# Kernel tuning notes

Measured on AMD Instinct MI355X. Metric: run time of the kernel, lower is better.

The kernel has to match this reference:

```python
import jax, jax.numpy as jnp
import numpy as np

NUM_FEAT = 1024
NUM_GROUP = 16
DIM_K = NUM_FEAT // NUM_GROUP  # 64
FEAT_DIM = 64
WAVE_LENGTH = 1000.0


def position_embedding(box, ctx_box):
    # box: (M,4), ctx_box: (N,4) corner encoding -> (M*N, 64)
    xmin, ymin, xmax, ymax = jnp.split(box, 4, axis=1)            # (M,1) each
    bw = xmax - xmin + 1.0
    bh = ymax - ymin + 1.0
    cx = 0.5 * (xmin + xmax)
    cy = 0.5 * (ymin + ymax)
    cxmin, cymin, cxmax, cymax = jnp.split(ctx_box, 4, axis=1)    # (N,1) each
    cbw = cxmax - cxmin + 1.0
    cbh = cymax - cymin + 1.0
    ccx = 0.5 * (cxmin + cxmax)
    ccy = 0.5 * (cymin + cymax)
    dx = jnp.log(jnp.clip(jnp.abs((cx - ccx.T) / bw), 1e-3))      # (M,N)
    dy = jnp.log(jnp.clip(jnp.abs((cy - ccy.T) / bh), 1e-3))
    dw = jnp.log(cbw.T / bw)
    dh = jnp.log(cbh.T / bh)
    pos = jnp.stack((dx, dy, dw, dh), axis=2)                     # (M,N,4)
    feat_range = jnp.arange(FEAT_DIM // 8, dtype=jnp.float32)     # (8,)
    dim_mat = jnp.power(jnp.float32(WAVE_LENGTH), (8.0 / FEAT_DIM) * feat_range)
    div = (100.0 * pos)[..., None] / dim_mat                      # (M,N,4,8)
    emb = jnp.concatenate((jnp.sin(div), jnp.cos(div)), axis=3)   # (M,N,4,16)
    M, N = pos.shape[0], pos.shape[1]
    return emb.reshape(M * N, FEAT_DIM)


def setup_inputs() -> dict:
    key = jax.random.key(0)
    ks = jax.random.split(key, 12)
    M, N = 512, 1024

    def make_boxes(k, n):
        k1, k2 = jax.random.split(k)
        xy = jax.random.uniform(k1, (n, 2), dtype=jnp.float32) * 800.0
        wh = jax.random.uniform(k2, (n, 2), dtype=jnp.float32) * 200.0 + 1.0
        return jnp.concatenate([xy, xy + wh], axis=1)             # valid corners

    return {
        "feat": jax.random.normal(ks[0], (M, NUM_FEAT), dtype=jnp.float32),
        "ctx_feat": jax.random.normal(ks[1], (N, NUM_FEAT), dtype=jnp.float32),
        "box": make_boxes(ks[2], M),
        "ctx_box": make_boxes(ks[3], N),
        # torch Linear stores weight as (out, in); apply as x @ W.T + b
        "w_fc_gt": jax.random.normal(ks[4], (NUM_FEAT, 1024), dtype=jnp.float32) * 0.01,
        "b_fc_gt": jnp.zeros((NUM_FEAT,), dtype=jnp.float32),
        "w_fc_ctx": jax.random.normal(ks[5], (NUM_FEAT, 1024), dtype=jnp.float32) * 0.01,
        "b_fc_ctx": jnp.zeros((NUM_FEAT,), dtype=jnp.float32),
        "w_pos_gt": jax.random.normal(ks[6], (NUM_GROUP, FEAT_DIM), dtype=jnp.float32) * 0.01,
        "b_pos_gt": jnp.zeros((NUM_GROUP,), dtype=jnp.float32),
        "w_pos_ctx": jax.random.normal(ks[7], (NUM_GROUP, FEAT_DIM), dtype=jnp.float32) * 0.01,
        "b_pos_ctx": jnp.zeros((NUM_GROUP,), dtype=jnp.float32),
        # grouped 1x1 conv (16384 -> 1024, groups=16): per-group weight (64 out, 1024 in)
        "w_conv": jax.random.normal(ks[8], (NUM_GROUP, DIM_K, NUM_FEAT), dtype=jnp.float32) * 0.02,
        "b_conv": jnp.zeros((NUM_FEAT,), dtype=jnp.float32),
    }


def reference(feat, ctx_feat, box, ctx_box,
              w_fc_gt, b_fc_gt, w_fc_ctx, b_fc_ctx,
              w_pos_gt, b_pos_gt, w_pos_ctx, b_pos_ctx,
              w_conv, b_conv):
    M, N = feat.shape[0], ctx_feat.shape[0]
    # positional bias per group: (M*N,64) -relu-> linear -> (G,M,N)
    pe_gt = jax.nn.relu(position_embedding(box, ctx_box))
    pos_gt = (pe_gt @ w_pos_gt.T + b_pos_gt).T.reshape(NUM_GROUP, M, N)
    pe_ctx = jax.nn.relu(position_embedding(ctx_box, box))
    pos_ctx = (pe_ctx @ w_pos_ctx.T + b_pos_ctx).T.reshape(NUM_GROUP, N, M)
    # grouped projections
    q = (feat @ w_fc_gt.T + b_fc_gt).reshape(M, NUM_GROUP, DIM_K)
    k = (ctx_feat @ w_fc_ctx.T + b_fc_ctx).reshape(N, NUM_GROUP, DIM_K)
    scores = jnp.einsum('mgd,ngd->gmn', q, k) / np.float32(np.sqrt(DIM_K))  # (G,M,N)
    # gt <- ctx attention with log-position bias
    w1 = jax.nn.softmax(jnp.log(jnp.clip(pos_gt, 1e-6)) + scores, axis=-1)  # (G,M,N)
    att1 = jnp.einsum('gmn,nc->mgc', w1, ctx_feat)                          # (M,G,1024)
    out_gt = jnp.einsum('mgc,goc->mgo', att1, w_conv).reshape(M, NUM_FEAT) + b_conv
    # ctx <- gt attention (note: original module reuses gt_ctx_linear_out here)
    w2 = jax.nn.softmax(jnp.log(jnp.clip(pos_ctx, 1e-6)) + scores.transpose(0, 2, 1), axis=-1)  # (G,N,M)
    att2 = jnp.einsum('gnm,mc->ngc', w2, feat)                              # (N,G,1024)
    out_ctx = jnp.einsum('ngc,goc->ngo', att2, w_conv).reshape(N, NUM_FEAT) + b_conv
    return out_gt, out_ctx
```

## Files before the change

### kernel.cpp

```cpp
#include <hip/hip_runtime.h>
#include <math.h>


typedef __attribute__((ext_vector_type(8))) short short8;
typedef __attribute__((ext_vector_type(4))) float floatx4;
typedef __attribute__((ext_vector_type(4))) _Float16 half4;
typedef __attribute__((ext_vector_type(4))) unsigned uint4v;

__device__ inline unsigned short f32_bf16_rne(float x) {
    union { float f; unsigned u; } v; v.f = x;
    unsigned u = v.u;
    return (unsigned short)((u + 0x7fffu + ((u >> 16) & 1u)) >> 16);
}

__device__ inline unsigned fbits(float x) {
    union { float f; unsigned u; } v; v.f = x; return v.u;
}
__device__ inline float bitsf(unsigned u) {
    union { unsigned u; float f; } v; v.u = u; return v.f;
}

__device__ __forceinline__ floatx4 mfma16(short8 a, short8 b, floatx4 c) {
    return __builtin_amdgcn_mfma_f32_16x16x32_bf16(a, b, c, 0, 0, 0);
}

__device__ __forceinline__ void gemm_tile_pack(
    const unsigned short* __restrict__ Ab, int lda,
    const unsigned short* __restrict__ Bb, int ldb, int K,
    unsigned short* __restrict__ out_base,
    const float* __restrict__ biasvec,
    unsigned short* As, unsigned short* Bs)
{
    const int tid = threadIdx.x;
    const int lr = tid >> 3;
    const int lk = (tid & 7) * 8;
    const int lane = tid & 63;
    const int wave = tid >> 6;
    const int qr = (wave >> 1) * 32;
    const int qc = (wave & 1) * 32;
    const int m = lane & 15;
    const int quad = lane >> 4;

    const unsigned short* Ap  = Ab + (long long)lr * lda + lk;
    const unsigned short* Ap2 = Ap + 32LL * lda;
    const unsigned short* Bp  = Bb + (long long)lr * ldb + lk;
    const unsigned short* Bp2 = Bp + 32LL * ldb;
    unsigned short* AsW  = As + lr * 72 + lk;
    unsigned short* AsW2 = As + (lr + 32) * 72 + lk;
    unsigned short* BsW  = Bs + lr * 72 + lk;
    unsigned short* BsW2 = Bs + (lr + 32) * 72 + lk;
    const unsigned short* a0p = As + (qr + m) * 72 + quad * 8;
    const unsigned short* b0p = Bs + (qc + m) * 72 + quad * 8;

    floatx4 acc00 = {0.f,0.f,0.f,0.f}, acc01 = {0.f,0.f,0.f,0.f};
    floatx4 acc10 = {0.f,0.f,0.f,0.f}, acc11 = {0.f,0.f,0.f,0.f};

    int4 pa0 = *(const int4*)Ap;
    int4 pa1 = *(const int4*)Ap2;
    int4 pb0 = *(const int4*)Bp;
    int4 pb1 = *(const int4*)Bp2;
    int4 qa0 = *(const int4*)(Ap + 64);
    int4 qa1 = *(const int4*)(Ap2 + 64);
    int4 qb0 = *(const int4*)(Bp + 64);
    int4 qb1 = *(const int4*)(Bp2 + 64);

    for (int k0 = 0; ; ) {
        __syncthreads();
        *(int4*)AsW  = pa0;
        *(int4*)AsW2 = pa1;
        *(int4*)BsW  = pb0;
        *(int4*)BsW2 = pb1;
        __syncthreads();
        pa0 = qa0; pa1 = qa1; pb0 = qb0; pb1 = qb1;
        const int kf = k0 + 128;
        if (kf < K) {
            qa0 = *(const int4*)(Ap + kf);
            qa1 = *(const int4*)(Ap2 + kf);
            qb0 = *(const int4*)(Bp + kf);
            qb1 = *(const int4*)(Bp2 + kf);
        }
        #pragma unroll
        for (int kk = 0; kk < 64; kk += 32) {
            short8 a0 = *(const short8*)(a0p + kk);
            short8 a1 = *(const short8*)(a0p + 16 * 72 + kk);
            short8 b0 = *(const short8*)(b0p + kk);
            short8 b1 = *(const short8*)(b0p + 16 * 72 + kk);
            acc00 = mfma16(a0, b0, acc00);
            acc01 = mfma16(a0, b1, acc01);
            acc10 = mfma16(a1, b0, acc10);
            acc11 = mfma16(a1, b1, acc11);
        }
        k0 += 64;
        if (k0 >= K) break;
    }

    float bias0 = 0.f, bias1 = 0.f;
    if (biasvec) { bias0 = biasvec[qc + m]; bias1 = biasvec[qc + 16 + m]; }

    __syncthreads();
    const floatx4 accs[2][2] = { {acc00, acc01}, {acc10, acc11} };
    #pragma unroll
    for (int i = 0; i < 2; ++i)
        #pragma unroll
        for (int r = 0; r < 4; ++r) {
            const int lrow = qr + i * 16 + quad * 4 + r;
            #pragma unroll
            for (int j = 0; j < 2; ++j) {
                const int lcol = qc + j * 16 + m;
                float val = accs[i][j][r] + (j ? bias1 : bias0);
                As[lrow * 72 + lcol] = f32_bf16_rne(val);
            }
        }
    __syncthreads();
    #pragma unroll
    for (int h = 0; h < 2; ++h) {
        const int f = h * 2048 + tid * 8;
        const int lanep = (f >> 3) & 63;
        const int part = (f >> 9) & 1;
        const int ploc = f >> 10;
        const int row = ploc * 16 + (lanep & 15);
        const int col = part * 32 + ((lanep >> 4) << 3);
        short8 v8 = *(const short8*)&As[row * 72 + col];
        *(short8*)(out_base + f) = v8;
    }
}

__global__ __launch_bounds__(256) void projvt_kernel(
    const unsigned short* __restrict__ in_bf, const unsigned short* __restrict__ wgt,
    const unsigned short* __restrict__ wctx,
    const float* __restrict__ bgt, const float* __restrict__ bctx,
    unsigned short* __restrict__ qk_pack,
    const unsigned short* __restrict__ wconv, unsigned short* __restrict__ vt_pack)
{
    __shared__ __align__(16) unsigned short As[64 * 72];
    __shared__ __align__(16) unsigned short Bs[64 * 72];
    if (blockIdx.z == 0) {
        const int bm = blockIdx.x * 64;
        const int g = blockIdx.y;
        const unsigned short* B = (bm < 512) ? wgt : wctx;
        const float* bias = (bm < 512) ? bgt : bctx;
        gemm_tile_pack(in_bf + (long long)bm * 1024, 1024,
                       B + (long long)g * 65536, 1024, 1024,
                       qk_pack + ((long long)g * 96 + blockIdx.x * 4) * 1024,
                       bias + g * 64, As, Bs);
    } else {
        const int cc = blockIdx.x;
        const int g = blockIdx.y;
        gemm_tile_pack(wconv + (long long)g * 65536, 1024,
                       in_bf + (long long)cc * 65536, 1024, 1024,
                       vt_pack + ((long long)g * 24 + cc) * 4096,
                       nullptr, As, Bs);
    }
}

__global__ __launch_bounds__(256) void prep_kernel(
    const float* __restrict__ box, const float* __restrict__ ctx_box,
    const float* __restrict__ w_gt, const float* __restrict__ b_gt,
    const float* __restrict__ w_ctx, const float* __restrict__ b_ctx,
    _Float16* __restrict__ bias_gt, _Float16* __restrict__ bias_ctx,
    const float* s0, unsigned short* d0, int n0,
    const float* s1, unsigned short* d1, int n1,
    const float* s2, unsigned short* d2, int n2,
    const float* s3, unsigned short* d3, int n3,
    const float* s4, unsigned short* d4, int n4)
{
    const int bx = blockIdx.x;
    if (bx >= 16384) {
        const int bc = bx - 16384;
        const int which = bc >> 10;
        const int xb = bc & 1023;
        const float* s; unsigned short* d; int n;
        switch (which) {
            case 0: s = s0; d = d0; n = n0; break;
            case 1: s = s1; d = d1; n = n1; break;
            case 2: s = s2; d = d2; n = n2; break;
            case 3: s = s3; d = d3; n = n3; break;
            default: s = s4; d = d4; n = n4; break;
        }
        int idx = (xb * 256 + threadIdx.x) * 4;
        if (idx < n) {
            float4 v = *(const float4*)(s + idx);
            ushort4 o;
            o.x = f32_bf16_rne(v.x); o.y = f32_bf16_rne(v.y);
            o.z = f32_bf16_rne(v.z); o.w = f32_bf16_rne(v.w);
            *(ushort4*)(d + idx) = o;
        }
        return;
    }

    const bool first = (bx < 8192);
    const long long blk = first ? bx : (bx - 8192);
    const float* boxA = first ? box : ctx_box;
    const float* boxB = first ? ctx_box : box;
    const float* w_pos = first ? w_gt : w_ctx;
    const float* b_pos = first ? b_gt : b_ctx;
    _Float16* out = first ? bias_gt : bias_ctx;
    const int shift = first ? 10 : 9;

    __shared__ __align__(16) unsigned short BsH[16 * 72];
    __shared__ __align__(16) unsigned short BsL[16 * 72];
    __shared__ _Float16 stg[16 * 68];

    const int tid = threadIdx.x;

    {
        const int g = tid >> 4;
        const int d = (tid & 15) * 4;
        float4 wv = *(const float4*)(w_pos + g * 64 + d);
        unsigned u0 = fbits(wv.x), u1 = fbits(wv.y);
        unsigned u2 = fbits(wv.z), u3 = fbits(wv.w);
        unsigned r0 = fbits(wv.x - bitsf(u0 & 0xFFFF0000u));
        unsigned r1 = fbits(wv.y - bitsf(u1 & 0xFFFF0000u));
        unsigned r2 = fbits(wv.z - bitsf(u2 & 0xFFFF0000u));
        unsigned r3 = fbits(wv.w - bitsf(u3 & 0xFFFF0000u));
        uint2 hv, lv;
        hv.x = (u0 >> 16) | (u1 & 0xFFFF0000u);
        hv.y = (u2 >> 16) | (u3 & 0xFFFF0000u);
        lv.x = (r0 >> 16) | (r1 & 0xFFFF0000u);
        lv.y = (r2 >> 16) | (r3 & 0xFFFF0000u);
        *(uint2*)&BsH[g * 72 + d] = hv;
        *(uint2*)&BsL[g * 72 + d] = lv;
    }
    __syncthreads();

    const int lane = tid & 63;
    const int w = tid >> 6;
    const int m = lane & 15;
    const int quad = lane >> 4;
    const long long pbase = blk * 64;

    const long long pair = pbase + w * 16 + m;
    const int i = (int)(pair >> shift);
    const int j = (int)(pair & ((1 << shift) - 1));
    float4 ba = *(const float4*)(boxA + i * 4);
    float4 bb = *(const float4*)(boxB + j * 4);
    float bw = ba.z - ba.x + 1.f, bh = ba.w - ba.y + 1.f;
    float cx = 0.5f * (ba.x + ba.z), cy = 0.5f * (ba.y + ba.w);
    float cbw = bb.z - bb.x + 1.f, cbh = bb.w - bb.y + 1.f;
    float ccx = 0.5f * (bb.x + bb.z), ccy = 0.5f * (bb.y + bb.w);
    const bool qlow = (quad < 2);
    float arg_lo = qlow ? fmaxf(fabsf((cx - ccx) / bw), 1e-3f)
                        : fmaxf(fabsf((cy - ccy) / bh), 1e-3f);
    float arg_hi = qlow ? (cbw / bw) : (cbh / bh);
    float pos_lo = __logf(arg_lo);
    float pos_hi = __logf(arg_hi);
    const float phase = (quad & 1) ? 1.57079632679f : 0.0f;

    const float w100[8] = {100.f, 42.169650342f, 17.782794100f, 7.498942093f,
                           3.162277660f, 1.333521432f, 0.562341325f, 0.237137371f};
    unsigned hp0[4], lp0[4], hp1[4], lp1[4];
    #pragma unroll
    for (int fi = 0; fi < 4; ++fi) {
        float x0 = fmaxf(__sinf(fmaf(w100[2*fi],     pos_lo, phase)), 0.f);
        float x1 = fmaxf(__sinf(fmaf(w100[2*fi + 1], pos_lo, phase)), 0.f);
        unsigned u0 = fbits(x0), u1 = fbits(x1);
        unsigned r0 = fbits(x0 - bitsf(u0 & 0xFFFF0000u));
        unsigned r1 = fbits(x1 - bitsf(u1 & 0xFFFF0000u));
        hp0[fi] = (u0 >> 16) | (u1 & 0xFFFF0000u);
        lp0[fi] = (r0 >> 16) | (r1 & 0xFFFF0000u);
        float y0 = fmaxf(__sinf(fmaf(w100[2*fi],     pos_hi, phase)), 0.f);
        float y1 = fmaxf(__sinf(fmaf(w100[2*fi + 1], pos_hi, phase)), 0.f);
        unsigned v0 = fbits(y0), v1 = fbits(y1);
        unsigned s0r = fbits(y0 - bitsf(v0 & 0xFFFF0000u));
        unsigned s1r = fbits(y1 - bitsf(v1 & 0xFFFF0000u));
        hp1[fi] = (v0 >> 16) | (v1 & 0xFFFF0000u);
        lp1[fi] = (s0r >> 16) | (s1r & 0xFFFF0000u);
    }
    union { uint4v u; short8 s; } cH0, cL0, cH1, cL1;
    cH0.u = (uint4v){hp0[0], hp0[1], hp0[2], hp0[3]};
    cL0.u = (uint4v){lp0[0], lp0[1], lp0[2], lp0[3]};
    cH1.u = (uint4v){hp1[0], hp1[1], hp1[2], hp1[3]};
    cL1.u = (uint4v){lp1[0], lp1[1], lp1[2], lp1[3]};

    const unsigned short* bpH = &BsH[m * 72 + quad * 8];
    const unsigned short* bpL = &BsL[m * 72 + quad * 8];
    short8 bH0 = *(const short8*)bpH;
    short8 bH1 = *(const short8*)(bpH + 32);
    short8 bL0 = *(const short8*)bpL;
    short8 bL1 = *(const short8*)(bpL + 32);

    floatx4 acc = {0.f, 0.f, 0.f, 0.f};
    acc = mfma16(cH0.s, bH0, acc);
    acc = mfma16(cH1.s, bH1, acc);
    acc = mfma16(cH0.s, bL0, acc);
    acc = mfma16(cH1.s, bL1, acc);
    acc = mfma16(cL0.s, bH0, acc);
    acc = mfma16(cL1.s, bH1, acc);

    const float bpv = b_pos[m];
    #pragma unroll
    for (int r = 0; r < 4; ++r)
        stg[m * 68 + w * 16 + quad * 4 + r] = (_Float16)__logf(fmaxf(acc[r] + bpv, 1e-6f));
    __syncthreads();
    const int g2 = tid >> 4, c16 = tid & 15;
    *(half4*)(out + (long long)g2 * 524288 + pbase + c16 * 4) =
        *(const half4*)&stg[g2 * 68 + c16 * 4];
}

template <int NC>
__device__ __forceinline__ void attn_body(
    int g, int bx,
    const unsigned short* __restrict__ qk, int pA, int pB0,
    const _Float16* __restrict__ bias,
    const unsigned short* __restrict__ vt, int cc0,
    const float* __restrict__ b_conv, float* __restrict__ outp,
    unsigned short* wpack, float* redA, float* redB)
{
    constexpr int NCOL = NC * 64;
    constexpr int WS = NCOL + 8;
    constexpr int SHIFT = (NC == 16) ? 10 : 9;

    const int bm = bx * 16;
    const int tid = threadIdx.x;
    const int lane = tid & 63;
    const int w = tid >> 6;
    const int m = lane & 15;
    const int quad = lane >> 4;

    _Float16* bb = (_Float16*)wpack;
    {
        const _Float16* bsrc = bias + (long long)g * 524288 + (long long)bm * NCOL;
        #pragma unroll
        for (int i = 0; i < (16 * NCOL) / (256 * 8); ++i) {
            const int idx = (i * 256 + tid) * 8;
            const int row = idx >> SHIFT;
            const int col = idx & (NCOL - 1);
            *(int4*)(bb + row * WS + col) = *(const int4*)(bsrc + idx);
        }
    }

    const unsigned short* abase = qk + ((long long)(g * 96 + pA)) * 1024;
    short8 aq0 = *(const short8*)(abase + lane * 8);
    short8 aq1 = *(const short8*)(abase + 512 + lane * 8);

    const unsigned short* bptr = qk + ((long long)(g * 96 + pB0 + w)) * 1024 + lane * 8;
    short8 B0[2], B1[2];
    B0[0] = *(const short8*)bptr;
    B1[0] = *(const short8*)(bptr + 512);
    B0[1] = *(const short8*)(bptr + 4096);
    B1[1] = *(const short8*)(bptr + 4096 + 512);

    __syncthreads();

    const _Float16* brow = bb + (quad * 4) * WS + w * 16 + m;

    float v[NC][4];
    #pragma unroll
    for (int c = 0; c < NC; ++c) {
        float bv[4];
        #pragma unroll
        for (int r = 0; r < 4; ++r)
            bv[r] = (float)brow[r * WS + c * 64];
        floatx4 acc = {0.f, 0.f, 0.f, 0.f};
        acc = mfma16(aq0, B0[c & 1], acc);
        acc = mfma16(aq1, B1[c & 1], acc);
        if (c + 2 < NC) {
            const unsigned short* nb = bptr + (long long)(c + 2) * 4096;
            B0[c & 1] = *(const short8*)nb;
            B1[c & 1] = *(const short8*)(nb + 512);
        }
        #pragma unroll
        for (int r = 0; r < 4; ++r)
            v[c][r] = fmaf(0.125f, acc[r], bv[r]);
    }

    const unsigned short* vptr = vt + ((long long)(g * 24 + cc0)) * 4096
                               + w * 1024 + lane * 8;
    short8 V0[2], V1[2];
    V0[0] = *(const short8*)vptr;
    V1[0] = *(const short8*)(vptr + 512);
    V0[1] = *(const short8*)(vptr + 4096);
    V1[1] = *(const short8*)(vptr + 4096 + 512);

    float rmax[4];
    #pragma unroll
    for (int r = 0; r < 4; ++r) {
        float mx = v[0][r];
        #pragma unroll
        for (int c = 1; c < NC; ++c) mx = fmaxf(mx, v[c][r]);
        #pragma unroll
        for (int off = 1; off < 16; off <<= 1)
            mx = fmaxf(mx, __shfl_xor(mx, off, 64));
        rmax[r] = mx;
    }
    if (m == 0) {
        #pragma unroll
        for (int r = 0; r < 4; ++r) redA[w * 16 + quad * 4 + r] = rmax[r];
    }
    __syncthreads();
    #pragma unroll
    for (int r = 0; r < 4; ++r)
        rmax[r] = fmaxf(fmaxf(redA[quad*4+r], redA[16 + quad*4+r]),
                        fmaxf(redA[32 + quad*4+r], redA[48 + quad*4+r]));

    float rsum[4] = {0.f, 0.f, 0.f, 0.f};
    #pragma unroll
    for (int c = 0; c < NC; ++c)
        #pragma unroll
        for (int r = 0; r < 4; ++r) {
            v[c][r] = __expf(v[c][r] - rmax[r]);
            rsum[r] += v[c][r];
        }
    #pragma unroll
    for (int r = 0; r < 4; ++r)
        #pragma unroll
        for (int off = 1; off < 16; off <<= 1)
            rsum[r] += __shfl_xor(rsum[r], off, 64);
    if (m == 0) {
        #pragma unroll
        for (int r = 0; r < 4; ++r) redB[w * 16 + quad * 4 + r] = rsum[r];
    }
    __syncthreads();
    float rinv[4];
    #pragma unroll
    for (int r = 0; r < 4; ++r)
        rinv[r] = 1.f / (redB[quad*4+r] + redB[16 + quad*4+r] +
                         redB[32 + quad*4+r] + redB[48 + quad*4+r]);

    #pragma unroll
    for (int c = 0; c < NC; ++c)
        #pragma unroll
        for (int r = 0; r < 4; ++r)
            wpack[(quad * 4 + r) * WS + c * 64 + w * 16 + m] =
                f32_bf16_rne(v[c][r] * rinv[r]);

    __syncthreads();

    floatx4 oacc = {0.f, 0.f, 0.f, 0.f};
    const unsigned short* awp = wpack + m * WS + quad * 8;
    #pragma unroll
    for (int kc = 0; kc < NC; ++kc) {
        short8 a0 = *(const short8*)(awp + kc * 64);
        short8 a1 = *(const short8*)(awp + kc * 64 + 32);
        oacc = mfma16(a0, V0[kc & 1], oacc);
        oacc = mfma16(a1, V1[kc & 1], oacc);
        if (kc + 2 < NC) {
            const unsigned short* nv = vptr + (long long)(kc + 2) * 4096;
            V0[kc & 1] = *(const short8*)nv;
            V1[kc & 1] = *(const short8*)(nv + 512);
        }
    }

    const int o = w * 16 + m;
    const float bc = b_conv[g * 64 + o];
    __syncthreads();
    float* ot = (float*)wpack;
    #pragma unroll
    for (int r = 0; r < 4; ++r)
        ot[(quad * 4 + r) * 68 + o] = oacc[r] + bc;
    __syncthreads();
    const int orow = tid >> 4, oc4 = (tid & 15) * 4;
    float4 ov = *(const float4*)&ot[orow * 68 + oc4];
    *(float4*)(outp + (long long)(bm + orow) * 1024 + g * 64 + oc4) = ov;
}

__global__ __launch_bounds__(256) void attn_out_kernel(
    const unsigned short* __restrict__ qk_pack,
    const _Float16* __restrict__ bias_gt, const _Float16* __restrict__ bias_ctx,
    const unsigned short* __restrict__ vt_pack, const float* __restrict__ b_conv,
    float* __restrict__ out_gt, float* __restrict__ out_ctx)
{
    __shared__ __align__(16) unsigned short wpack[16 * 1032];
    __shared__ float redA[64], redB[64];

    const int bx = blockIdx.x;
    if (bx < 512) {
        const int rb = bx & 31;
        attn_body<16>(bx >> 5, rb, qk_pack, rb, 32,
                      bias_gt, vt_pack, 8, b_conv, out_gt,
                      wpack, redA, redB);
    } else {
        const int b2 = bx - 512;
        const int rb = b2 & 63;
        attn_body<8>(b2 >> 6, rb, qk_pack, 32 + rb, 0,
                     bias_ctx, vt_pack, 0, b_conv, out_ctx,
                     wpack, redA, redB);
    }
}

extern "C" void kernel_launch(void* const* d_in, const int* in_sizes, int n_in,
                              void* d_out, int out_size, void* d_ws, size_t ws_size,
                              hipStream_t stream)
{
    const float* feat     = (const float*)d_in[0];
    const float* ctx_feat = (const float*)d_in[1];
    const float* box      = (const float*)d_in[2];
    const float* ctx_box  = (const float*)d_in[3];
    const float* w_fc_gt  = (const float*)d_in[4];
    const float* b_fc_gt  = (const float*)d_in[5];
    const float* w_fc_ctx = (const float*)d_in[6];
    const float* b_fc_ctx = (const float*)d_in[7];
    const float* w_pos_gt = (const float*)d_in[8];
    const float* b_pos_gt = (const float*)d_in[9];
    const float* w_pos_ctx= (const float*)d_in[10];
    const float* b_pos_ctx= (const float*)d_in[11];
    const float* w_conv   = (const float*)d_in[12];
    const float* b_conv   = (const float*)d_in[13];

    float* ws = (float*)d_ws;
    unsigned short* in_bf   = (unsigned short*)ws;
    unsigned short* ctx_bf  = in_bf + 524288LL;
    unsigned short* qk_pack = in_bf + 1572864LL;
    _Float16* bias_gt  = (_Float16*)(ws + 1572864LL);
    _Float16* bias_ctx = (_Float16*)(ws + 5767168LL);
    unsigned short* wconv_bf = (unsigned short*)(ws + 9961472LL);
    unsigned short* vt_pack  = (unsigned short*)(ws + 10485760LL);
    unsigned short* wfcgt_bf = (unsigned short*)(ws + 11272192LL);
    unsigned short* wfcctx_bf= wfcgt_bf + 1048576LL;

    float* out_gt  = (float*)d_out;
    float* out_ctx = (float*)d_out + 524288LL;

    hipLaunchKernelGGL(prep_kernel, dim3(21504), dim3(256), 0, stream,
                       box, ctx_box, w_pos_gt, b_pos_gt, w_pos_ctx, b_pos_ctx,
                       bias_gt, bias_ctx,
                       feat, in_bf, 524288,
                       ctx_feat, ctx_bf, 1048576,
                       w_fc_gt, wfcgt_bf, 1048576,
                       w_fc_ctx, wfcctx_bf, 1048576,
                       w_conv, wconv_bf, 1048576);

    hipLaunchKernelGGL(projvt_kernel, dim3(24, 16, 2), dim3(256), 0, stream,
                       in_bf, wfcgt_bf, wfcctx_bf, b_fc_gt, b_fc_ctx, qk_pack,
                       wconv_bf, vt_pack);

    hipLaunchKernelGGL(attn_out_kernel, dim3(1536), dim3(256), 0, stream,
                       qk_pack, bias_gt, bias_ctx, vt_pack, b_conv, out_gt, out_ctx);
}
```

Baseline: 156.6 us.

## Process four pair tiles per block and dedupe position-log computation via LDS

The position-bias part of the prep kernel now has each block loop over four 64-pair tiles instead of one, which cuts the grid from 21504 to 9216 blocks. The block's weight split into bf16 hi/lo parts in LDS is now reused across the four tiles. The four log-position values per pair are computed once by distinct threads with fast reciprocals and shared through LDS, replacing the redundant divisions and logs done in each quad lane. This adds extra barriers per iteration and gives less parallelism per launch.

```diff
diff --git a/kernel.cpp b/kernel.cpp
--- a/kernel.cpp
+++ b/kernel.cpp
@@ -165,8 +165,8 @@
     const float* s4, unsigned short* d4, int n4)
 {
     const int bx = blockIdx.x;
-    if (bx >= 16384) {
-        const int bc = bx - 16384;
+    if (bx >= 4096) {
+        const int bc = bx - 4096;
         const int which = bc >> 10;
         const int xb = bc & 1023;
         const float* s; unsigned short* d; int n;
@@ -188,8 +188,8 @@
         return;
     }
 
-    const bool first = (bx < 8192);
-    const long long blk = first ? bx : (bx - 8192);
+    const bool first = (bx < 2048);
+    const long long blk = first ? bx : (bx - 2048);
     const float* boxA = first ? box : ctx_box;
     const float* boxB = first ? ctx_box : box;
     const float* w_pos = first ? w_gt : w_ctx;
@@ -199,6 +199,7 @@
 
     __shared__ __align__(16) unsigned short BsH[16 * 72];
     __shared__ __align__(16) unsigned short BsL[16 * 72];
+    __shared__ float posL[4 * 68];
     __shared__ _Float16 stg[16 * 68];
 
     const int tid = threadIdx.x;
@@ -227,50 +228,9 @@
     const int w = tid >> 6;
     const int m = lane & 15;
     const int quad = lane >> 4;
-    const long long pbase = blk * 64;
-
-    const long long pair = pbase + w * 16 + m;
-    const int i = (int)(pair >> shift);
-    const int j = (int)(pair & ((1 << shift) - 1));
-    float4 ba = *(const float4*)(boxA + i * 4);
-    float4 bb = *(const float4*)(boxB + j * 4);
-    float bw = ba.z - ba.x + 1.f, bh = ba.w - ba.y + 1.f;
-    float cx = 0.5f * (ba.x + ba.z), cy = 0.5f * (ba.y + ba.w);
-    float cbw = bb.z - bb.x + 1.f, cbh = bb.w - bb.y + 1.f;
-    float ccx = 0.5f * (bb.x + bb.z), ccy = 0.5f * (bb.y + bb.w);
     const bool qlow = (quad < 2);
-    float arg_lo = qlow ? fmaxf(fabsf((cx - ccx) / bw), 1e-3f)
-                        : fmaxf(fabsf((cy - ccy) / bh), 1e-3f);
-    float arg_hi = qlow ? (cbw / bw) : (cbh / bh);
-    float pos_lo = __logf(arg_lo);
-    float pos_hi = __logf(arg_hi);
     const float phase = (quad & 1) ? 1.57079632679f : 0.0f;
-
-    const float w100[8] = {100.f, 42.169650342f, 17.782794100f, 7.498942093f,
-                           3.162277660f, 1.333521432f, 0.562341325f, 0.237137371f};
-    unsigned hp0[4], lp0[4], hp1[4], lp1[4];
-    #pragma unroll
-    for (int fi = 0; fi < 4; ++fi) {
-        float x0 = fmaxf(__sinf(fmaf(w100[2*fi],     pos_lo, phase)), 0.f);
-        float x1 = fmaxf(__sinf(fmaf(w100[2*fi + 1], pos_lo, phase)), 0.f);
-        unsigned u0 = fbits(x0), u1 = fbits(x1);
-        unsigned r0 = fbits(x0 - bitsf(u0 & 0xFFFF0000u));
-        unsigned r1 = fbits(x1 - bitsf(u1 & 0xFFFF0000u));
-        hp0[fi] = (u0 >> 16) | (u1 & 0xFFFF0000u);
-        lp0[fi] = (r0 >> 16) | (r1 & 0xFFFF0000u);
-        float y0 = fmaxf(__sinf(fmaf(w100[2*fi],     pos_hi, phase)), 0.f);
-        float y1 = fmaxf(__sinf(fmaf(w100[2*fi + 1], pos_hi, phase)), 0.f);
-        unsigned v0 = fbits(y0), v1 = fbits(y1);
-        unsigned s0r = fbits(y0 - bitsf(v0 & 0xFFFF0000u));
-        unsigned s1r = fbits(y1 - bitsf(v1 & 0xFFFF0000u));
-        hp1[fi] = (v0 >> 16) | (v1 & 0xFFFF0000u);
-        lp1[fi] = (s0r >> 16) | (s1r & 0xFFFF0000u);
-    }
-    union { uint4v u; short8 s; } cH0, cL0, cH1, cL1;
-    cH0.u = (uint4v){hp0[0], hp0[1], hp0[2], hp0[3]};
-    cL0.u = (uint4v){lp0[0], lp0[1], lp0[2], lp0[3]};
-    cH1.u = (uint4v){hp1[0], hp1[1], hp1[2], hp1[3]};
-    cL1.u = (uint4v){lp1[0], lp1[1], lp1[2], lp1[3]};
+    const float bpv = b_pos[m];
 
     const unsigned short* bpH = &BsH[m * 72 + quad * 8];
     const unsigned short* bpL = &BsL[m * 72 + quad * 8];
@@ -279,22 +239,85 @@
     short8 bL0 = *(const short8*)bpL;
     short8 bL1 = *(const short8*)(bpL + 32);
 
-    floatx4 acc = {0.f, 0.f, 0.f, 0.f};
-    acc = mfma16(cH0.s, bH0, acc);
-    acc = mfma16(cH1.s, bH1, acc);
-    acc = mfma16(cH0.s, bL0, acc);
-    acc = mfma16(cH1.s, bL1, acc);
-    acc = mfma16(cL0.s, bH0, acc);
-    acc = mfma16(cL1.s, bH1, acc);
-
-    const float bpv = b_pos[m];
-    #pragma unroll
-    for (int r = 0; r < 4; ++r)
-        stg[m * 68 + w * 16 + quad * 4 + r] = (_Float16)__logf(fmaxf(acc[r] + bpv, 1e-6f));
-    __syncthreads();
-    const int g2 = tid >> 4, c16 = tid & 15;
-    *(half4*)(out + (long long)g2 * 524288 + pbase + c16 * 4) =
-        *(const half4*)&stg[g2 * 68 + c16 * 4];
+    const float w100[8] = {100.f, 42.169650342f, 17.782794100f, 7.498942093f,
+                           3.162277660f, 1.333521432f, 0.562341325f, 0.237137371f};
+    const long long pbase = blk * 256;
+
+    for (int it = 0; it < 4; ++it) {
+        const long long pb = pbase + it * 64;
+
+        {
+            const int pl = tid & 63;
+            const int p = tid >> 6;
+            const long long pair = pb + pl;
+            const int i = (int)(pair >> shift);
+            const int j = (int)(pair & ((1 << shift) - 1));
+            float4 ba = *(const float4*)(boxA + i * 4);
+            float4 bb = *(const float4*)(boxB + j * 4);
+            float posv;
+            if (p == 0) {
+                float r = __builtin_amdgcn_rcpf(ba.z - ba.x + 1.f);
+                posv = __logf(fmaxf(fabsf((0.5f*(ba.x+ba.z) - 0.5f*(bb.x+bb.z)) * r), 1e-3f));
+            } else if (p == 1) {
+                float r = __builtin_amdgcn_rcpf(ba.w - ba.y + 1.f);
+                posv = __logf(fmaxf(fabsf((0.5f*(ba.y+ba.w) - 0.5f*(bb.y+bb.w)) * r), 1e-3f));
+            } else if (p == 2) {
+                float r = __builtin_amdgcn_rcpf(ba.z - ba.x + 1.f);
+                posv = __logf((bb.z - bb.x + 1.f) * r);
+            } else {
+                float r = __builtin_amdgcn_rcpf(ba.w - ba.y + 1.f);
+                posv = __logf((bb.w - bb.y + 1.f) * r);
+            }
+            posL[p * 68 + pl] = posv;
+        }
+        __syncthreads();
+
+        const int plB = w * 16 + m;
+        const float pos_lo = posL[(qlow ? 0 : 1) * 68 + plB];
+        const float pos_hi = posL[(qlow ? 2 : 3) * 68 + plB];
+
+        unsigned hp0[4], lp0[4], hp1[4], lp1[4];
+        #pragma unroll
+        for (int fi = 0; fi < 4; ++fi) {
+            float x0 = fmaxf(__sinf(fmaf(w100[2*fi],     pos_lo, phase)), 0.f);
+            float x1 = fmaxf(__sinf(fmaf(w100[2*fi + 1], pos_lo, phase)), 0.f);
+            unsigned u0 = fbits(x0), u1 = fbits(x1);
+            unsigned r0 = fbits(x0 - bitsf(u0 & 0xFFFF0000u));
+            unsigned r1 = fbits(x1 - bitsf(u1 & 0xFFFF0000u));
+            hp0[fi] = (u0 >> 16) | (u1 & 0xFFFF0000u);
+            lp0[fi] = (r0 >> 16) | (r1 & 0xFFFF0000u);
+            float y0 = fmaxf(__sinf(fmaf(w100[2*fi],     pos_hi, phase)), 0.f);
+            float y1 = fmaxf(__sinf(fmaf(w100[2*fi + 1], pos_hi, phase)), 0.f);
+            unsigned v0 = fbits(y0), v1 = fbits(y1);
+            unsigned s0r = fbits(y0 - bitsf(v0 & 0xFFFF0000u));
+            unsigned s1r = fbits(y1 - bitsf(v1 & 0xFFFF0000u));
+            hp1[fi] = (v0 >> 16) | (v1 & 0xFFFF0000u);
+            lp1[fi] = (s0r >> 16) | (s1r & 0xFFFF0000u);
+        }
+        union { uint4v u; short8 s; } cH0, cL0, cH1, cL1;
+        cH0.u = (uint4v){hp0[0], hp0[1], hp0[2], hp0[3]};
+        cL0.u = (uint4v){lp0[0], lp0[1], lp0[2], lp0[3]};
+        cH1.u = (uint4v){hp1[0], hp1[1], hp1[2], hp1[3]};
+        cL1.u = (uint4v){lp1[0], lp1[1], lp1[2], lp1[3]};
+
+        floatx4 acc = {0.f, 0.f, 0.f, 0.f};
+        acc = mfma16(cH0.s, bH0, acc);
+        acc = mfma16(cH1.s, bH1, acc);
+        acc = mfma16(cH0.s, bL0, acc);
+        acc = mfma16(cH1.s, bL1, acc);
+        acc = mfma16(cL0.s, bH0, acc);
+        acc = mfma16(cL1.s, bH1, acc);
+
+        #pragma unroll
+        for (int r = 0; r < 4; ++r)
+            stg[m * 68 + w * 16 + quad * 4 + r] =
+                (_Float16)__logf(fmaxf(acc[r] + bpv, 1e-6f));
+        __syncthreads();
+
+        const int g2 = tid >> 4, c16 = tid & 15;
+        *(half4*)(out + (long long)g2 * 524288 + pb + c16 * 4) =
+            *(const half4*)&stg[g2 * 68 + c16 * 4];
+    }
 }
 
 template <int NC>
@@ -511,7 +534,7 @@
     float* out_gt  = (float*)d_out;
     float* out_ctx = (float*)d_out + 524288LL;
 
-    hipLaunchKernelGGL(prep_kernel, dim3(21504), dim3(256), 0, stream,
+    hipLaunchKernelGGL(prep_kernel, dim3(9216), dim3(256), 0, stream,
                        box, ctx_box, w_pos_gt, b_pos_gt, w_pos_ctx, b_pos_ctx,
                        bias_gt, bias_ctx,
                        feat, in_bf, 524288,
```

After: 149.8 us. 4.3% less time.
